# Kernel tuning notes

Measured on AMD Instinct MI355X. Metric: run time of the kernel, lower is better.

Reference implementation:

```python
import jax, jax.numpy as jnp
import numpy as np

NH = 8       # num attention heads (hardcoded in module)
NL = 6       # n_layers
EPS = 1e-5   # LayerNorm eps (torch default)


def pos_enc(dim, length):
    # faithful to module's positional_encoding: even cols sin, odd cols cos,
    # with angle = pos / 10000^(2i/dim) where i indexes ALL columns via arange(0,2*dim,2)/dim
    pos = jnp.arange(length, dtype=jnp.float32)[:, None]
    div = 1.0 / (10000.0 ** (jnp.arange(0, 2 * dim, 2, dtype=jnp.float32) / dim))
    ang = pos * div[None, :]  # [length, dim]
    cols = jnp.arange(dim)
    return jnp.where(cols % 2 == 0, jnp.sin(ang), jnp.cos(ang))


def layernorm(x):
    m = x.mean(-1, keepdims=True)
    v = x.var(-1, keepdims=True)  # biased, matches torch LayerNorm
    return (x - m) / jnp.sqrt(v + EPS)


def setup_inputs() -> dict:
    key = jax.random.key(0)
    ks = jax.random.split(key, 8)
    S, H = 2048, 1024
    D = H // NH
    sc = 1.0 / np.sqrt(H)  # ~ torch Linear init scale
    return {
        "inputs": jax.random.normal(ks[0], (S, H), jnp.float32),
        "Wq": jax.random.normal(ks[1], (NH, H, D), jnp.float32) * sc,
        "bq": jnp.zeros((NH, D), jnp.float32),
        "Wk": jax.random.normal(ks[2], (NH, H, D), jnp.float32) * sc,
        "bk": jnp.zeros((NH, D), jnp.float32),
        "Wv": jax.random.normal(ks[3], (NH, H, D), jnp.float32) * sc,
        "bv": jnp.zeros((NH, D), jnp.float32),
        "W1": jax.random.normal(ks[4], (H, H), jnp.float32) * sc,
        "b1": jnp.zeros((H,), jnp.float32),
        "W2": jax.random.normal(ks[5], (H, H), jnp.float32) * sc,
        "b2": jnp.zeros((H,), jnp.float32),
    }


def reference(inputs, Wq, bq, Wk, bk, Wv, bv, W1, b1, W2, b2):
    S, H = inputs.shape
    scale = jnp.sqrt(jnp.float32(H))  # module scales by sqrt(hidden), not sqrt(head_dim)
    x = inputs + pos_enc(H, S)        # [S, H]
    kv = x  # dropout in eval mode = identity; k_v_input fixed to layer-0 input (faithful)
    # K/V are identical every layer (shared weights + fixed kv input)
    K = jnp.einsum('sh,nhd->nsd', kv, Wk) + bk[:, None, :]  # [NH, S, D]
    V = jnp.einsum('sh,nhd->nsd', kv, Wv) + bv[:, None, :]
    t_in = x
    for _ in range(NL):
        Q = jnp.einsum('sh,nhd->nsd', t_in, Wq) + bq[:, None, :]
        A = jax.nn.softmax(jnp.einsum('nsd,ntd->nst', Q, K) / scale, axis=-1)
        ctx = jnp.einsum('nst,ntd->nsd', A, V)        # [NH, S, D]
        cat = ctx.transpose(1, 0, 2).reshape(S, H)    # concat heads on feature dim
        mh = layernorm(t_in + cat)
        ff = jax.nn.relu(mh @ W1 + b1) @ W2 + b2
        t_in = layernorm(mh + ff)
    return t_in
```

## Files before the change

### kernel.cpp

```cpp
#include <hip/hip_runtime.h>

#define S_LEN 2048
#define H_DIM 1024
#define NHEAD 8
#define D_HEAD 128
#define KSPLIT 2
#define KV_PER (S_LEN / KSPLIT)

typedef __bf16 bf16x8 __attribute__((ext_vector_type(8)));
typedef float floatx4 __attribute__((ext_vector_type(4)));

__device__ __forceinline__ float b2f(unsigned short u) {
    union { unsigned int i; float f; } v;
    v.i = ((unsigned int)u) << 16;
    return v.f;
}
__device__ __forceinline__ unsigned short f2b(float f) {
    union { float f; unsigned int i; } v;
    v.f = f;
    return (unsigned short)((v.i + 0x7fffu + ((v.i >> 16) & 1u)) >> 16);
}

__device__ __forceinline__ void dma16(void* lds, const void* g) {
    __builtin_amdgcn_global_load_lds(
        (const __attribute__((address_space(1))) void*)g,
        (__attribute__((address_space(3))) void*)lds, 16, 0, 0);
}

__global__ __launch_bounds__(256) void posenc_kernel(
    const float* __restrict__ in, float* __restrict__ xf,
    unsigned short* __restrict__ xb)
{
    int g = blockIdx.x * 256 + threadIdx.x;
    int s = g >> 10;
    int h = g & 1023;
    float dv = powf(10000.0f, -(float)h * (1.0f / 512.0f));
    float ang = (float)s * dv;
    float pe = (h & 1) ? cosf(ang) : sinf(ang);
    float x = in[g] + pe;
    xf[g] = x;
    xb[g] = f2b(x);
}

__global__ __launch_bounds__(256) void transpose_all(
    const float* __restrict__ Wq, const float* __restrict__ Wk,
    const float* __restrict__ Wv, const float* __restrict__ W1,
    const float* __restrict__ W2,
    unsigned short* __restrict__ WqT, unsigned short* __restrict__ WkT,
    unsigned short* __restrict__ WvT, unsigned short* __restrict__ W1T,
    unsigned short* __restrict__ W2T)
{
    __shared__ unsigned short tile[32][33];
    const int z = blockIdx.z;
    const float* ih;
    unsigned short* oh;
    int ldin;
    if (z < 8)       { ih = Wq + (size_t)z * 131072;        oh = WqT + (size_t)z * 131072;        ldin = 128; }
    else if (z < 16) { ih = Wk + (size_t)(z - 8) * 131072;  oh = WkT + (size_t)(z - 8) * 131072;  ldin = 128; }
    else if (z < 24) { ih = Wv + (size_t)(z - 16) * 131072; oh = WvT + (size_t)(z - 16) * 131072; ldin = 128; }
    else if (z < 32) { ih = W1 + (size_t)(z - 24) * 128;    oh = W1T + (size_t)(z - 24) * 131072; ldin = 1024; }
    else             { ih = W2 + (size_t)(z - 32) * 128;    oh = W2T + (size_t)(z - 32) * 131072; ldin = 1024; }
    const int r0 = blockIdx.y * 32, c0 = blockIdx.x * 32;
    const int tx = threadIdx.x, ty = threadIdx.y;
    for (int i = ty; i < 32; i += 8)
        tile[i][tx] = f2b(ih[(size_t)(r0 + i) * ldin + c0 + tx]);
    __syncthreads();
    for (int i = ty; i < 32; i += 8)
        oh[(size_t)(c0 + i) * 1024 + r0 + tx] = tile[tx][i];
}

template <int MODE, bool RELU>
__device__ __forceinline__ void gemm128_core(
    unsigned short* sA, unsigned short* sB,
    const unsigned short* A, const unsigned short* Bt,
    const float* bias, float* Cf, unsigned short* Cb, int ldt, int i0, int j0)
{
    const int K = H_DIM;
    const int tid = threadIdx.x;
    const int wave = tid >> 6, lane = tid & 63;
    const int quad = lane >> 4, l16 = lane & 15;
    const int wm = (wave >> 1) * 64, wn = (wave & 1) * 64;

    const int srow = lane >> 3;
    const int schunk = (lane & 7) ^ srow;
    const unsigned short* Ap = A + (size_t)(i0 + wave * 8 + srow) * K + schunk * 8;
    const unsigned short* Bp = Bt + (size_t)(j0 + wave * 8 + srow) * K + schunk * 8;

    floatx4 z4 = {0.f, 0.f, 0.f, 0.f};
    floatx4 acc[4][4];
#pragma unroll
    for (int i = 0; i < 4; i++)
#pragma unroll
        for (int j = 0; j < 4; j++) acc[i][j] = z4;

#pragma unroll
    for (int it = 0; it < 4; it++) {
        const int lb = (wave * 8 + it * 32) * 64;
        dma16(sA + lb, Ap + (size_t)(it * 32) * K);
        dma16(sB + lb, Bp + (size_t)(it * 32) * K);
    }
    __syncthreads();

    int buf = 0;
    for (int k0 = 0; k0 < K; k0 += 64) {
        if (k0 + 64 < K) {
            unsigned short* nA = sA + (buf ^ 1) * 8192;
            unsigned short* nB = sB + (buf ^ 1) * 8192;
#pragma unroll
            for (int it = 0; it < 4; it++) {
                const int lb = (wave * 8 + it * 32) * 64;
                dma16(nA + lb, Ap + (size_t)(it * 32) * K + k0 + 64);
                dma16(nB + lb, Bp + (size_t)(it * 32) * K + k0 + 64);
            }
        }
        const unsigned short* cA = sA + buf * 8192;
        const unsigned short* cB = sB + buf * 8192;
#pragma unroll
        for (int kh = 0; kh < 2; kh++) {
            bf16x8 af[4], bfr[4];
#pragma unroll
            for (int mi = 0; mi < 4; mi++) {
                int row = wm + mi * 16 + l16;
                int p = (kh * 4 + quad) ^ (l16 & 7);
                af[mi] = *(const bf16x8*)(cA + row * 64 + p * 8);
            }
#pragma unroll
            for (int ni = 0; ni < 4; ni++) {
                int row = wn + ni * 16 + l16;
                int p = (kh * 4 + quad) ^ (l16 & 7);
                bfr[ni] = *(const bf16x8*)(cB + row * 64 + p * 8);
            }
#pragma unroll
            for (int mi = 0; mi < 4; mi++)
#pragma unroll
                for (int ni = 0; ni < 4; ni++)
                    acc[mi][ni] = __builtin_amdgcn_mfma_f32_16x16x32_bf16(
                        af[mi], bfr[ni], acc[mi][ni], 0, 0, 0);
        }
        __syncthreads();
        buf ^= 1;
    }

#pragma unroll
    for (int mi = 0; mi < 4; mi++) {
#pragma unroll
        for (int ni = 0; ni < 4; ni++) {
            const int col = j0 + wn + ni * 16 + l16;
            const float bval = bias[col];
#pragma unroll
            for (int r = 0; r < 4; r++) {
                const int row_o = i0 + wm + mi * 16 + quad * 4 + r;
                float v = acc[mi][ni][r] + bval;
                if (RELU) v = fmaxf(v, 0.0f);
                if (MODE == 0) Cb[(size_t)row_o * H_DIM + col] = f2b(v);
                else if (MODE == 1) Cb[(size_t)col * ldt + row_o] = f2b(v);
                else Cf[(size_t)row_o * H_DIM + col] = v;
            }
        }
    }
}

template <int MODE, bool RELU>
__global__ __launch_bounds__(256, 2) void gemm128(
    const unsigned short* __restrict__ A, const unsigned short* __restrict__ Bt,
    const float* __restrict__ bias, float* __restrict__ Cf,
    unsigned short* __restrict__ Cb, int ldt)
{
    extern __shared__ __align__(16) unsigned short gsm[];
    gemm128_core<MODE, RELU>(gsm, gsm + 16384, A, Bt, bias, Cf, Cb, ldt,
                             blockIdx.y * 128, blockIdx.x * 128);
}

__global__ __launch_bounds__(256, 2) void gemm_kv(
    const unsigned short* __restrict__ A,
    const unsigned short* __restrict__ WkT, const unsigned short* __restrict__ WvT,
    const float* __restrict__ bk, const float* __restrict__ bv,
    unsigned short* __restrict__ Kb, unsigned short* __restrict__ Vtb)
{
    extern __shared__ __align__(16) unsigned short gsm[];
    if (blockIdx.z == 0)
        gemm128_core<0, false>(gsm, gsm + 16384, A, WkT, bk, nullptr, Kb, 0,
                               blockIdx.y * 128, blockIdx.x * 128);
    else
        gemm128_core<1, false>(gsm, gsm + 16384, A, WvT, bv, nullptr, Vtb, S_LEN,
                               blockIdx.y * 128, blockIdx.x * 128);
}

__global__ __launch_bounds__(256, 2) void flash_attn(
    const unsigned short* __restrict__ Qg, const unsigned short* __restrict__ Kg,
    const unsigned short* __restrict__ Vt, unsigned short* __restrict__ Op,
    float* __restrict__ Lp)
{
    extern __shared__ __align__(16) unsigned short smem[];
    unsigned short* sK0 = smem;
    unsigned short* sV0 = smem + 16384;
    unsigned short* sP = smem + 32768;

    const int tid = threadIdx.x;
    const int wave = tid >> 6, lane = tid & 63;
    const int quad = lane >> 4, l16 = lane & 15;
    const int head = blockIdx.y;
    const int q0 = blockIdx.x * 64;
    const int split = blockIdx.z;
    const int h0 = head * D_HEAD;

    bf16x8 aq[4];
    const int qrow = q0 + wave * 16 + l16;
#pragma unroll
    for (int ks = 0; ks < 4; ks++)
        aq[ks] = *(const bf16x8*)(Qg + (size_t)qrow * H_DIM + h0 + ks * 32 + quad * 8);

    unsigned short* myP = sP + wave * (16 * 72);

    const int k_r = wave * 4 + (lane >> 4);
    const int k_c = (lane & 15) ^ (k_r & 15);
    const int v_r = wave * 8 + (lane >> 3);
    const int v_c = (lane & 7) ^ (v_r & 7);

    const unsigned short* Kbase = Kg + h0;
    const unsigned short* Vbase = Vt + (size_t)h0 * S_LEN;
    const int kt0 = split * KV_PER;

    floatx4 z4 = {0.f, 0.f, 0.f, 0.f};
    floatx4 o[8];
#pragma unroll
    for (int i = 0; i < 8; i++) o[i] = z4;
    float l_r[4] = {0.f, 0.f, 0.f, 0.f};

#pragma unroll
    for (int it = 0; it < 4; it++) {
        dma16(sK0 + (wave * 4 + it * 16) * 128,
              Kbase + (size_t)(kt0 + k_r + it * 16) * H_DIM + k_c * 8);
        dma16(sV0 + (wave * 8 + it * 32) * 64,
              Vbase + (size_t)(v_r + it * 32) * S_LEN + kt0 + v_c * 8);
    }
    __syncthreads();

    int buf = 0;
    for (int it0 = 0; it0 < KV_PER; it0 += 64) {
        const int t0 = kt0 + it0;
        if (it0 + 64 < KV_PER) {
            const int nt = t0 + 64;
            unsigned short* nK = sK0 + (buf ^ 1) * 8192;
            unsigned short* nV = sV0 + (buf ^ 1) * 8192;
#pragma unroll
            for (int it = 0; it < 4; it++) {
                dma16(nK + (wave * 4 + it * 16) * 128,
                      Kbase + (size_t)(nt + k_r + it * 16) * H_DIM + k_c * 8);
                dma16(nV + (wave * 8 + it * 32) * 64,
                      Vbase + (size_t)(v_r + it * 32) * S_LEN + nt + v_c * 8);
            }
        }
        const unsigned short* cK = sK0 + buf * 8192;
        const unsigned short* cV = sV0 + buf * 8192;

        floatx4 sc[4];
#pragma unroll
        for (int ni = 0; ni < 4; ni++) {
            sc[ni] = z4;
#pragma unroll
            for (int ks = 0; ks < 4; ks++) {
                int p = (ks * 4 + quad) ^ l16;
                bf16x8 bk = *(const bf16x8*)(cK + (ni * 16 + l16) * 128 + p * 8);
                sc[ni] = __builtin_amdgcn_mfma_f32_16x16x32_bf16(aq[ks], bk, sc[ni], 0, 0, 0);
            }
        }

#pragma unroll
        for (int ni = 0; ni < 4; ni++)
#pragma unroll
            for (int r = 0; r < 4; r++) {
                float p = __expf(sc[ni][r] * 0.03125f);
                sc[ni][r] = p;
                l_r[r] += p;
            }

#pragma unroll
        for (int ni = 0; ni < 4; ni++)
#pragma unroll
            for (int r = 0; r < 4; r++) {
                int prow = quad * 4 + r;
                myP[prow * 72 + ((ni * 16 + l16) ^ ((prow & 8) << 1))] = f2b(sc[ni][r]);
            }
        bf16x8 ap[2];
#pragma unroll
        for (int ks = 0; ks < 2; ks++)
            ap[ks] = *(const bf16x8*)(myP + l16 * 72 + ((ks * 32 + quad * 8) ^ ((l16 & 8) << 1)));

#pragma unroll
        for (int ni = 0; ni < 8; ni++) {
#pragma unroll
            for (int ks = 0; ks < 2; ks++) {
                int p = (ks * 4 + quad) ^ (l16 & 7);
                bf16x8 bv = *(const bf16x8*)(cV + (ni * 16 + l16) * 64 + p * 8);
                o[ni] = __builtin_amdgcn_mfma_f32_16x16x32_bf16(ap[ks], bv, o[ni], 0, 0, 0);
            }
        }

        __syncthreads();
        buf ^= 1;
    }

#pragma unroll
    for (int r = 0; r < 4; r++)
#pragma unroll
        for (int off = 1; off < 16; off <<= 1)
            l_r[r] += __shfl_xor(l_r[r], off, 64);

#pragma unroll
    for (int r = 0; r < 4; r++) {
        float inv = 1.0f / l_r[r];
        int row = q0 + wave * 16 + quad * 4 + r;
#pragma unroll
        for (int ni = 0; ni < 8; ni++)
            Op[((size_t)split * S_LEN + row) * H_DIM + h0 + ni * 16 + l16] =
                f2b(o[ni][r] * inv);
        if (l16 == 0)
            Lp[(split * NHEAD + head) * S_LEN + row] = l_r[r];
    }
}

__global__ __launch_bounds__(256) void merge_add_layernorm(
    const float* __restrict__ t, const unsigned short* __restrict__ Op,
    const float* __restrict__ Lp,
    float* __restrict__ of, unsigned short* __restrict__ ob)
{
    __shared__ float red[8];
    const int row = blockIdx.x, tid = threadIdx.x;
    const int head = tid >> 5;
    const size_t base = (size_t)row * H_DIM + tid * 4;

    float l_s[KSPLIT];
    ushort4 os[KSPLIT];
#pragma unroll
    for (int sp = 0; sp < KSPLIT; sp++) {
        os[sp] = *(const ushort4*)(Op + ((size_t)sp * S_LEN + row) * H_DIM + tid * 4);
        l_s[sp] = Lp[(sp * NHEAD + head) * S_LEN + row];
    }
    float W = 0.f, a0 = 0.f, a1 = 0.f, a2 = 0.f, a3 = 0.f;
#pragma unroll
    for (int sp = 0; sp < KSPLIT; sp++) {
        float w = l_s[sp];
        W += w;
        a0 += w * b2f(os[sp].x);
        a1 += w * b2f(os[sp].y);
        a2 += w * b2f(os[sp].z);
        a3 += w * b2f(os[sp].w);
    }
    float inv = 1.0f / W;
    float4 x = *(const float4*)(t + base);
    float v0 = x.x + a0 * inv, v1 = x.y + a1 * inv;
    float v2 = x.z + a2 * inv, v3 = x.w + a3 * inv;

    float s = v0 + v1 + v2 + v3;
    float q = v0 * v0 + v1 * v1 + v2 * v2 + v3 * v3;
#pragma unroll
    for (int off = 32; off >= 1; off >>= 1) {
        s += __shfl_xor(s, off, 64);
        q += __shfl_xor(q, off, 64);
    }
    if ((tid & 63) == 0) { red[tid >> 6] = s; red[4 + (tid >> 6)] = q; }
    __syncthreads();
    s = red[0] + red[1] + red[2] + red[3];
    q = red[4] + red[5] + red[6] + red[7];
    const float mean = s * (1.0f / (float)H_DIM);
    const float var = q * (1.0f / (float)H_DIM) - mean * mean;
    const float rstd = rsqrtf(var + 1e-5f);
    float o0 = (v0 - mean) * rstd, o1 = (v1 - mean) * rstd;
    float o2 = (v2 - mean) * rstd, o3 = (v3 - mean) * rstd;
    *(float4*)(of + base) = make_float4(o0, o1, o2, o3);
    *(ushort4*)(ob + base) = make_ushort4(f2b(o0), f2b(o1), f2b(o2), f2b(o3));
}

__global__ __launch_bounds__(256) void add_layernorm(
    const float* __restrict__ a, const float* __restrict__ b,
    float* __restrict__ of, unsigned short* __restrict__ ob)
{
    __shared__ float red[8];
    const int row = blockIdx.x, tid = threadIdx.x;
    const size_t base = (size_t)row * H_DIM + tid * 4;
    float4 x = *(const float4*)(a + base);
    float4 y = *(const float4*)(b + base);
    float v0 = x.x + y.x, v1 = x.y + y.y, v2 = x.z + y.z, v3 = x.w + y.w;
    float s = v0 + v1 + v2 + v3;
    float q = v0 * v0 + v1 * v1 + v2 * v2 + v3 * v3;
#pragma unroll
    for (int off = 32; off >= 1; off >>= 1) {
        s += __shfl_xor(s, off, 64);
        q += __shfl_xor(q, off, 64);
    }
    if ((tid & 63) == 0) { red[tid >> 6] = s; red[4 + (tid >> 6)] = q; }
    __syncthreads();
    s = red[0] + red[1] + red[2] + red[3];
    q = red[4] + red[5] + red[6] + red[7];
    const float mean = s * (1.0f / (float)H_DIM);
    const float var = q * (1.0f / (float)H_DIM) - mean * mean;
    const float rstd = rsqrtf(var + 1e-5f);
    float o0 = (v0 - mean) * rstd, o1 = (v1 - mean) * rstd;
    float o2 = (v2 - mean) * rstd, o3 = (v3 - mean) * rstd;
    *(float4*)(of + base) = make_float4(o0, o1, o2, o3);
    *(ushort4*)(ob + base) = make_ushort4(f2b(o0), f2b(o1), f2b(o2), f2b(o3));
}

extern "C" void kernel_launch(void* const* d_in, const int* in_sizes, int n_in,
                              void* d_out, int out_size, void* d_ws, size_t ws_size,
                              hipStream_t stream)
{
    (void)in_sizes; (void)n_in; (void)out_size; (void)ws_size;
    const float* in = (const float*)d_in[0];
    const float* Wq = (const float*)d_in[1];
    const float* bq = (const float*)d_in[2];
    const float* Wk = (const float*)d_in[3];
    const float* bk = (const float*)d_in[4];
    const float* Wv = (const float*)d_in[5];
    const float* bv = (const float*)d_in[6];
    const float* W1 = (const float*)d_in[7];
    const float* b1 = (const float*)d_in[8];
    const float* W2 = (const float*)d_in[9];
    const float* b2 = (const float*)d_in[10];

    char* ws = (char*)d_ws;
    const size_t MB = 1024 * 1024;
    float* t_f32 = (float*)(ws + 0 * MB);
    float* cf_f32 = (float*)(ws + 8 * MB);
    unsigned short* t_b = (unsigned short*)(ws + 16 * MB);
    unsigned short* K_b = (unsigned short*)(ws + 20 * MB);
    unsigned short* Vt_b = (unsigned short*)(ws + 24 * MB);
    unsigned short* Q_b = (unsigned short*)(ws + 28 * MB);
    unsigned short* WqT = (unsigned short*)(ws + 32 * MB);
    unsigned short* WkT = (unsigned short*)(ws + 34 * MB);
    unsigned short* WvT = (unsigned short*)(ws + 36 * MB);
    unsigned short* W1T = (unsigned short*)(ws + 38 * MB);
    unsigned short* W2T = (unsigned short*)(ws + 40 * MB);
    unsigned short* Op = (unsigned short*)(ws + 42 * MB);
    float* Lp = (float*)(ws + 58 * MB);

    (void)hipFuncSetAttribute(reinterpret_cast<const void*>(&flash_attn),
                              hipFuncAttributeMaxDynamicSharedMemorySize, 74752);
    (void)hipFuncSetAttribute(reinterpret_cast<const void*>(&gemm128<0, false>),
                              hipFuncAttributeMaxDynamicSharedMemorySize, 65536);
    (void)hipFuncSetAttribute(reinterpret_cast<const void*>(&gemm128<0, true>),
                              hipFuncAttributeMaxDynamicSharedMemorySize, 65536);
    (void)hipFuncSetAttribute(reinterpret_cast<const void*>(&gemm128<2, false>),
                              hipFuncAttributeMaxDynamicSharedMemorySize, 65536);
    (void)hipFuncSetAttribute(reinterpret_cast<const void*>(&gemm_kv),
                              hipFuncAttributeMaxDynamicSharedMemorySize, 65536);

    transpose_all<<<dim3(4, 32, 40), dim3(32, 8), 0, stream>>>(
        Wq, Wk, Wv, W1, W2, WqT, WkT, WvT, W1T, W2T);

    posenc_kernel<<<(S_LEN * H_DIM) / 256, 256, 0, stream>>>(in, t_f32, t_b);

    dim3 gg(H_DIM / 128, S_LEN / 128);
    gemm_kv<<<dim3(8, 16, 2), 256, 65536, stream>>>(t_b, WkT, WvT, bk, bv, K_b, Vt_b);

    for (int layer = 0; layer < 6; layer++) {
        gemm128<0, false><<<gg, 256, 65536, stream>>>(t_b, WqT, bq, nullptr, Q_b, 0);
        flash_attn<<<dim3(S_LEN / 64, NHEAD, KSPLIT), 256, 74752, stream>>>(Q_b, K_b, Vt_b, Op, Lp);
        merge_add_layernorm<<<S_LEN, 256, 0, stream>>>(t_f32, Op, Lp, t_f32, t_b);
        gemm128<0, true><<<gg, 256, 65536, stream>>>(t_b, W1T, b1, nullptr, Q_b, 0);
        gemm128<2, false><<<gg, 256, 65536, stream>>>(Q_b, W2T, b2, cf_f32, nullptr, 0);
        float* of = (layer == 5) ? (float*)d_out : t_f32;
        add_layernorm<<<S_LEN, 256, 0, stream>>>(t_f32, cf_f32, of, t_b);
    }
}
```

Before: 593.9 us.

## Repartition flash attention work so waves split KV columns instead of query rows

Each wave now holds Q fragments for all 64 query rows and computes scores against its own 16 KV columns, then writes P to a shared block-wide tile. After a block barrier, each wave reads the full P tile and computes a 32-column slice of the output over all 64 rows. The aim is to cut per-wave LDS reads of K and V, since each K/V fragment is loaded once and reused across four MFMAs. In exchange it adds an extra __syncthreads per KV tile, a cross-wave reduction of row sums through LDS, more Q registers per wave and slightly more shared memory.

```diff
diff --git a/kernel.cpp b/kernel.cpp
--- a/kernel.cpp
+++ b/kernel.cpp
@@ -195,6 +195,7 @@
     unsigned short* sK0 = smem;
     unsigned short* sV0 = smem + 16384;
     unsigned short* sP = smem + 32768;
+    float* lsum = (float*)(smem + 32768 + 4608);
 
     const int tid = threadIdx.x;
     const int wave = tid >> 6, lane = tid & 63;
@@ -204,13 +205,14 @@
     const int split = blockIdx.z;
     const int h0 = head * D_HEAD;
 
-    bf16x8 aq[4];
-    const int qrow = q0 + wave * 16 + l16;
-#pragma unroll
-    for (int ks = 0; ks < 4; ks++)
-        aq[ks] = *(const bf16x8*)(Qg + (size_t)qrow * H_DIM + h0 + ks * 32 + quad * 8);
-
-    unsigned short* myP = sP + wave * (16 * 72);
+    bf16x8 aq[4][4];
+#pragma unroll
+    for (int mi = 0; mi < 4; mi++) {
+        const int qrow = q0 + mi * 16 + l16;
+#pragma unroll
+        for (int ks = 0; ks < 4; ks++)
+            aq[mi][ks] = *(const bf16x8*)(Qg + (size_t)qrow * H_DIM + h0 + ks * 32 + quad * 8);
+    }
 
     const int k_r = wave * 4 + (lane >> 4);
     const int k_c = (lane & 15) ^ (k_r & 15);
@@ -222,10 +224,16 @@
     const int kt0 = split * KV_PER;
 
     floatx4 z4 = {0.f, 0.f, 0.f, 0.f};
-    floatx4 o[8];
-#pragma unroll
-    for (int i = 0; i < 8; i++) o[i] = z4;
-    float l_r[4] = {0.f, 0.f, 0.f, 0.f};
+    floatx4 o[4][2];
+#pragma unroll
+    for (int mi = 0; mi < 4; mi++)
+#pragma unroll
+        for (int ni = 0; ni < 2; ni++) o[mi][ni] = z4;
+    float l_r[4][4];
+#pragma unroll
+    for (int mi = 0; mi < 4; mi++)
+#pragma unroll
+        for (int r = 0; r < 4; r++) l_r[mi][r] = 0.f;
 
 #pragma unroll
     for (int it = 0; it < 4; it++) {
@@ -256,44 +264,57 @@
 
         floatx4 sc[4];
 #pragma unroll
-        for (int ni = 0; ni < 4; ni++) {
-            sc[ni] = z4;
-#pragma unroll
-            for (int ks = 0; ks < 4; ks++) {
-                int p = (ks * 4 + quad) ^ l16;
-                bf16x8 bk = *(const bf16x8*)(cK + (ni * 16 + l16) * 128 + p * 8);
-                sc[ni] = __builtin_amdgcn_mfma_f32_16x16x32_bf16(aq[ks], bk, sc[ni], 0, 0, 0);
-            }
-        }
-
-#pragma unroll
-        for (int ni = 0; ni < 4; ni++)
+        for (int mi = 0; mi < 4; mi++) sc[mi] = z4;
+#pragma unroll
+        for (int ks = 0; ks < 4; ks++) {
+            int p = (ks * 4 + quad) ^ l16;
+            bf16x8 bk = *(const bf16x8*)(cK + (wave * 16 + l16) * 128 + p * 8);
+#pragma unroll
+            for (int mi = 0; mi < 4; mi++)
+                sc[mi] = __builtin_amdgcn_mfma_f32_16x16x32_bf16(
+                    aq[mi][ks], bk, sc[mi], 0, 0, 0);
+        }
+
+#pragma unroll
+        for (int mi = 0; mi < 4; mi++)
 #pragma unroll
             for (int r = 0; r < 4; r++) {
-                float p = __expf(sc[ni][r] * 0.03125f);
-                sc[ni][r] = p;
-                l_r[r] += p;
-            }
-
-#pragma unroll
-        for (int ni = 0; ni < 4; ni++)
+                float p = __expf(sc[mi][r] * 0.03125f);
+                sc[mi][r] = p;
+                l_r[mi][r] += p;
+            }
+
+#pragma unroll
+        for (int mi = 0; mi < 4; mi++)
 #pragma unroll
             for (int r = 0; r < 4; r++) {
-                int prow = quad * 4 + r;
-                myP[prow * 72 + ((ni * 16 + l16) ^ ((prow & 8) << 1))] = f2b(sc[ni][r]);
-            }
-        bf16x8 ap[2];
-#pragma unroll
-        for (int ks = 0; ks < 2; ks++)
-            ap[ks] = *(const bf16x8*)(myP + l16 * 72 + ((ks * 32 + quad * 8) ^ ((l16 & 8) << 1)));
-
-#pragma unroll
-        for (int ni = 0; ni < 8; ni++) {
+                int q = mi * 16 + quad * 4 + r;
+                sP[q * 72 + ((wave * 16 + l16) ^ ((q & 8) << 1))] = f2b(sc[mi][r]);
+            }
+        __syncthreads();
+
+        bf16x8 bv[2][2];
+#pragma unroll
+        for (int ni = 0; ni < 2; ni++)
 #pragma unroll
             for (int ks = 0; ks < 2; ks++) {
                 int p = (ks * 4 + quad) ^ (l16 & 7);
-                bf16x8 bv = *(const bf16x8*)(cV + (ni * 16 + l16) * 64 + p * 8);
-                o[ni] = __builtin_amdgcn_mfma_f32_16x16x32_bf16(ap[ks], bv, o[ni], 0, 0, 0);
+                bv[ni][ks] = *(const bf16x8*)(
+                    cV + ((wave * 2 + ni) * 16 + l16) * 64 + p * 8);
+            }
+#pragma unroll
+        for (int mi = 0; mi < 4; mi++) {
+            int q = mi * 16 + l16;
+            bf16x8 pa0 = *(const bf16x8*)(
+                sP + q * 72 + ((quad * 8) ^ ((q & 8) << 1)));
+            bf16x8 pa1 = *(const bf16x8*)(
+                sP + q * 72 + ((32 + quad * 8) ^ ((q & 8) << 1)));
+#pragma unroll
+            for (int ni = 0; ni < 2; ni++) {
+                o[mi][ni] = __builtin_amdgcn_mfma_f32_16x16x32_bf16(
+                    pa0, bv[ni][0], o[mi][ni], 0, 0, 0);
+                o[mi][ni] = __builtin_amdgcn_mfma_f32_16x16x32_bf16(
+                    pa1, bv[ni][1], o[mi][ni], 0, 0, 0);
             }
         }
 
@@ -302,22 +323,37 @@
     }
 
 #pragma unroll
-    for (int r = 0; r < 4; r++)
-#pragma unroll
-        for (int off = 1; off < 16; off <<= 1)
-            l_r[r] += __shfl_xor(l_r[r], off, 64);
-
-#pragma unroll
-    for (int r = 0; r < 4; r++) {
-        float inv = 1.0f / l_r[r];
-        int row = q0 + wave * 16 + quad * 4 + r;
-#pragma unroll
-        for (int ni = 0; ni < 8; ni++)
-            Op[((size_t)split * S_LEN + row) * H_DIM + h0 + ni * 16 + l16] =
-                f2b(o[ni][r] * inv);
-        if (l16 == 0)
-            Lp[(split * NHEAD + head) * S_LEN + row] = l_r[r];
-    }
+    for (int mi = 0; mi < 4; mi++)
+#pragma unroll
+        for (int r = 0; r < 4; r++)
+#pragma unroll
+            for (int off = 1; off < 16; off <<= 1)
+                l_r[mi][r] += __shfl_xor(l_r[mi][r], off, 64);
+
+    if (l16 == 0) {
+#pragma unroll
+        for (int mi = 0; mi < 4; mi++)
+#pragma unroll
+            for (int r = 0; r < 4; r++)
+                lsum[wave * 64 + mi * 16 + quad * 4 + r] = l_r[mi][r];
+    }
+    __syncthreads();
+
+#pragma unroll
+    for (int mi = 0; mi < 4; mi++)
+#pragma unroll
+        for (int r = 0; r < 4; r++) {
+            const int ql = mi * 16 + quad * 4 + r;
+            const float ltot = lsum[ql] + lsum[64 + ql] + lsum[128 + ql] + lsum[192 + ql];
+            const float inv = 1.0f / ltot;
+            const int row = q0 + ql;
+#pragma unroll
+            for (int ni = 0; ni < 2; ni++)
+                Op[((size_t)split * S_LEN + row) * H_DIM + h0 + (wave * 2 + ni) * 16 + l16] =
+                    f2b(o[mi][ni][r] * inv);
+            if (wave == 0 && l16 == 0)
+                Lp[(split * NHEAD + head) * S_LEN + row] = ltot;
+        }
 }
 
 __global__ __launch_bounds__(256) void merge_add_layernorm(
@@ -436,7 +472,7 @@
     float* Lp = (float*)(ws + 58 * MB);
 
     (void)hipFuncSetAttribute(reinterpret_cast<const void*>(&flash_attn),
-                              hipFuncAttributeMaxDynamicSharedMemorySize, 74752);
+                              hipFuncAttributeMaxDynamicSharedMemorySize, 75776);
     (void)hipFuncSetAttribute(reinterpret_cast<const void*>(&gemm128<0, false>),
                               hipFuncAttributeMaxDynamicSharedMemorySize, 65536);
     (void)hipFuncSetAttribute(reinterpret_cast<const void*>(&gemm128<0, true>),
@@ -456,7 +492,7 @@
 
     for (int layer = 0; layer < 6; layer++) {
         gemm128<0, false><<<gg, 256, 65536, stream>>>(t_b, WqT, bq, nullptr, Q_b, 0);
-        flash_attn<<<dim3(S_LEN / 64, NHEAD, KSPLIT), 256, 74752, stream>>>(Q_b, K_b, Vt_b, Op, Lp);
+        flash_attn<<<dim3(S_LEN / 64, NHEAD, KSPLIT), 256, 75776, stream>>>(Q_b, K_b, Vt_b, Op, Lp);
         merge_add_layernorm<<<S_LEN, 256, 0, stream>>>(t_f32, Op, Lp, t_f32, t_b);
         gemm128<0, true><<<gg, 256, 65536, stream>>>(t_b, W1T, b1, nullptr, Q_b, 0);
         gemm128<2, false><<<gg, 256, 65536, stream>>>(Q_b, W2T, b2, cf_f32, nullptr, 0);
```

After: 652.4 us. 1.1x slower.

## Split-K the Q-projection and FFN2 GEMMs, reducing partials in consumer kernels

Applied to the files above, without the earlier changes.

The Q projection and second FFN GEMM now run as split-K=2 launches of 256 blocks instead of 128, with each half writing fp32 partials. The partials are summed and biased in the consumers. Flash attention stages Q via LDS after adding both partials and bq, and a new add_layernorm3 sums the two W2 partials plus b2. This aims to fill more compute units on the 128-tile GEMMs. In exchange it adds fp32 partial-buffer writes and reads, plus an extra LDS pass and barrier in attention.

```diff
diff --git a/kernel.cpp b/kernel.cpp
--- a/kernel.cpp
+++ b/kernel.cpp
@@ -6,6 +6,7 @@
 #define D_HEAD 128
 #define KSPLIT 2
 #define KV_PER (S_LEN / KSPLIT)
+#define QP_ELEMS (S_LEN * H_DIM)
 
 typedef __bf16 bf16x8 __attribute__((ext_vector_type(8)));
 typedef float floatx4 __attribute__((ext_vector_type(4)));
@@ -69,13 +70,13 @@
         oh[(size_t)(c0 + i) * 1024 + r0 + tx] = tile[tx][i];
 }
 
-template <int MODE, bool RELU>
+template <int MODE, bool RELU, int KLEN>
 __device__ __forceinline__ void gemm128_core(
     unsigned short* sA, unsigned short* sB,
     const unsigned short* A, const unsigned short* Bt,
-    const float* bias, float* Cf, unsigned short* Cb, int ldt, int i0, int j0)
-{
-    const int K = H_DIM;
+    const float* bias, float* Cf, unsigned short* Cb, int ldt, int i0, int j0,
+    int kofs)
+{
     const int tid = threadIdx.x;
     const int wave = tid >> 6, lane = tid & 63;
     const int quad = lane >> 4, l16 = lane & 15;
@@ -83,8 +84,8 @@
 
     const int srow = lane >> 3;
     const int schunk = (lane & 7) ^ srow;
-    const unsigned short* Ap = A + (size_t)(i0 + wave * 8 + srow) * K + schunk * 8;
-    const unsigned short* Bp = Bt + (size_t)(j0 + wave * 8 + srow) * K + schunk * 8;
+    const unsigned short* Ap = A + (size_t)(i0 + wave * 8 + srow) * H_DIM + kofs + schunk * 8;
+    const unsigned short* Bp = Bt + (size_t)(j0 + wave * 8 + srow) * H_DIM + kofs + schunk * 8;
 
     floatx4 z4 = {0.f, 0.f, 0.f, 0.f};
     floatx4 acc[4][4];
@@ -96,21 +97,21 @@
 #pragma unroll
     for (int it = 0; it < 4; it++) {
         const int lb = (wave * 8 + it * 32) * 64;
-        dma16(sA + lb, Ap + (size_t)(it * 32) * K);
-        dma16(sB + lb, Bp + (size_t)(it * 32) * K);
+        dma16(sA + lb, Ap + (size_t)(it * 32) * H_DIM);
+        dma16(sB + lb, Bp + (size_t)(it * 32) * H_DIM);
     }
     __syncthreads();
 
     int buf = 0;
-    for (int k0 = 0; k0 < K; k0 += 64) {
-        if (k0 + 64 < K) {
+    for (int k0 = 0; k0 < KLEN; k0 += 64) {
+        if (k0 + 64 < KLEN) {
             unsigned short* nA = sA + (buf ^ 1) * 8192;
             unsigned short* nB = sB + (buf ^ 1) * 8192;
 #pragma unroll
             for (int it = 0; it < 4; it++) {
                 const int lb = (wave * 8 + it * 32) * 64;
-                dma16(nA + lb, Ap + (size_t)(it * 32) * K + k0 + 64);
-                dma16(nB + lb, Bp + (size_t)(it * 32) * K + k0 + 64);
+                dma16(nA + lb, Ap + (size_t)(it * 32) * H_DIM + k0 + 64);
+                dma16(nB + lb, Bp + (size_t)(it * 32) * H_DIM + k0 + 64);
             }
         }
         const unsigned short* cA = sA + buf * 8192;
@@ -146,7 +147,7 @@
 #pragma unroll
         for (int ni = 0; ni < 4; ni++) {
             const int col = j0 + wn + ni * 16 + l16;
-            const float bval = bias[col];
+            const float bval = (MODE == 3) ? 0.f : bias[col];
 #pragma unroll
             for (int r = 0; r < 4; r++) {
                 const int row_o = i0 + wm + mi * 16 + quad * 4 + r;
@@ -167,8 +168,19 @@
     unsigned short* __restrict__ Cb, int ldt)
 {
     extern __shared__ __align__(16) unsigned short gsm[];
-    gemm128_core<MODE, RELU>(gsm, gsm + 16384, A, Bt, bias, Cf, Cb, ldt,
-                             blockIdx.y * 128, blockIdx.x * 128);
+    gemm128_core<MODE, RELU, 1024>(gsm, gsm + 16384, A, Bt, bias, Cf, Cb, ldt,
+                                   blockIdx.y * 128, blockIdx.x * 128, 0);
+}
+
+__global__ __launch_bounds__(256, 2) void gemm_ks(
+    const unsigned short* __restrict__ A, const unsigned short* __restrict__ Bt,
+    float* __restrict__ Cp)
+{
+    extern __shared__ __align__(16) unsigned short gsm[];
+    float* Cf = Cp + (size_t)blockIdx.z * QP_ELEMS;
+    gemm128_core<3, false, 512>(gsm, gsm + 16384, A, Bt, nullptr, Cf, nullptr, 0,
+                                blockIdx.y * 128, blockIdx.x * 128,
+                                blockIdx.z * 512);
 }
 
 __global__ __launch_bounds__(256, 2) void gemm_kv(
@@ -179,17 +191,17 @@
 {
     extern __shared__ __align__(16) unsigned short gsm[];
     if (blockIdx.z == 0)
-        gemm128_core<0, false>(gsm, gsm + 16384, A, WkT, bk, nullptr, Kb, 0,
-                               blockIdx.y * 128, blockIdx.x * 128);
+        gemm128_core<0, false, 1024>(gsm, gsm + 16384, A, WkT, bk, nullptr, Kb, 0,
+                                     blockIdx.y * 128, blockIdx.x * 128, 0);
     else
-        gemm128_core<1, false>(gsm, gsm + 16384, A, WvT, bv, nullptr, Vtb, S_LEN,
-                               blockIdx.y * 128, blockIdx.x * 128);
+        gemm128_core<1, false, 1024>(gsm, gsm + 16384, A, WvT, bv, nullptr, Vtb, S_LEN,
+                                     blockIdx.y * 128, blockIdx.x * 128, 0);
 }
 
 __global__ __launch_bounds__(256, 2) void flash_attn(
-    const unsigned short* __restrict__ Qg, const unsigned short* __restrict__ Kg,
-    const unsigned short* __restrict__ Vt, unsigned short* __restrict__ Op,
-    float* __restrict__ Lp)
+    const float* __restrict__ Qp, const float* __restrict__ bq,
+    const unsigned short* __restrict__ Kg, const unsigned short* __restrict__ Vt,
+    unsigned short* __restrict__ Op, float* __restrict__ Lp)
 {
     extern __shared__ __align__(16) unsigned short smem[];
     unsigned short* sK0 = smem;
@@ -204,11 +216,39 @@
     const int split = blockIdx.z;
     const int h0 = head * D_HEAD;
 
+    unsigned short* LDSQ = smem;
+    {
+        const int r = tid >> 2;
+        const int cq = (tid & 3) * 32;
+        const float* q0p = Qp + (size_t)(q0 + r) * H_DIM + h0 + cq;
+        const float* q1p = q0p + QP_ELEMS;
+        const float* bqp = bq + head * D_HEAD + cq;
+#pragma unroll
+        for (int c = 0; c < 4; c++) {
+            float4 a0 = *(const float4*)(q0p + c * 8);
+            float4 a1 = *(const float4*)(q0p + c * 8 + 4);
+            float4 b0 = *(const float4*)(q1p + c * 8);
+            float4 b1 = *(const float4*)(q1p + c * 8 + 4);
+            float4 g0 = *(const float4*)(bqp + c * 8);
+            float4 g1 = *(const float4*)(bqp + c * 8 + 4);
+            ushort4 w0 = make_ushort4(f2b(a0.x + b0.x + g0.x), f2b(a0.y + b0.y + g0.y),
+                                      f2b(a0.z + b0.z + g0.z), f2b(a0.w + b0.w + g0.w));
+            ushort4 w1 = make_ushort4(f2b(a1.x + b1.x + g1.x), f2b(a1.y + b1.y + g1.y),
+                                      f2b(a1.z + b1.z + g1.z), f2b(a1.w + b1.w + g1.w));
+            *(ushort4*)(LDSQ + r * 136 + cq + c * 8) = w0;
+            *(ushort4*)(LDSQ + r * 136 + cq + c * 8 + 4) = w1;
+        }
+    }
+    __syncthreads();
+
     bf16x8 aq[4];
-    const int qrow = q0 + wave * 16 + l16;
-#pragma unroll
-    for (int ks = 0; ks < 4; ks++)
-        aq[ks] = *(const bf16x8*)(Qg + (size_t)qrow * H_DIM + h0 + ks * 32 + quad * 8);
+    {
+        const int qr = wave * 16 + l16;
+#pragma unroll
+        for (int ks = 0; ks < 4; ks++)
+            aq[ks] = *(const bf16x8*)(LDSQ + qr * 136 + ks * 32 + quad * 8);
+    }
+    __syncthreads();
 
     unsigned short* myP = sP + wave * (16 * 72);
 
@@ -372,16 +412,20 @@
     *(ushort4*)(ob + base) = make_ushort4(f2b(o0), f2b(o1), f2b(o2), f2b(o3));
 }
 
-__global__ __launch_bounds__(256) void add_layernorm(
-    const float* __restrict__ a, const float* __restrict__ b,
+__global__ __launch_bounds__(256) void add_layernorm3(
+    const float* __restrict__ a, const float* __restrict__ c2,
+    const float* __restrict__ b2,
     float* __restrict__ of, unsigned short* __restrict__ ob)
 {
     __shared__ float red[8];
     const int row = blockIdx.x, tid = threadIdx.x;
     const size_t base = (size_t)row * H_DIM + tid * 4;
     float4 x = *(const float4*)(a + base);
-    float4 y = *(const float4*)(b + base);
-    float v0 = x.x + y.x, v1 = x.y + y.y, v2 = x.z + y.z, v3 = x.w + y.w;
+    float4 y0 = *(const float4*)(c2 + base);
+    float4 y1 = *(const float4*)(c2 + QP_ELEMS + base);
+    float4 bb = *(const float4*)(b2 + tid * 4);
+    float v0 = x.x + y0.x + y1.x + bb.x, v1 = x.y + y0.y + y1.y + bb.y;
+    float v2 = x.z + y0.z + y1.z + bb.z, v3 = x.w + y0.w + y1.w + bb.w;
     float s = v0 + v1 + v2 + v3;
     float q = v0 * v0 + v1 * v1 + v2 * v2 + v3 * v3;
 #pragma unroll
@@ -422,26 +466,25 @@
     char* ws = (char*)d_ws;
     const size_t MB = 1024 * 1024;
     float* t_f32 = (float*)(ws + 0 * MB);
-    float* cf_f32 = (float*)(ws + 8 * MB);
-    unsigned short* t_b = (unsigned short*)(ws + 16 * MB);
-    unsigned short* K_b = (unsigned short*)(ws + 20 * MB);
-    unsigned short* Vt_b = (unsigned short*)(ws + 24 * MB);
-    unsigned short* Q_b = (unsigned short*)(ws + 28 * MB);
-    unsigned short* WqT = (unsigned short*)(ws + 32 * MB);
-    unsigned short* WkT = (unsigned short*)(ws + 34 * MB);
-    unsigned short* WvT = (unsigned short*)(ws + 36 * MB);
-    unsigned short* W1T = (unsigned short*)(ws + 38 * MB);
-    unsigned short* W2T = (unsigned short*)(ws + 40 * MB);
-    unsigned short* Op = (unsigned short*)(ws + 42 * MB);
-    float* Lp = (float*)(ws + 58 * MB);
+    unsigned short* t_b = (unsigned short*)(ws + 8 * MB);
+    unsigned short* K_b = (unsigned short*)(ws + 12 * MB);
+    unsigned short* Vt_b = (unsigned short*)(ws + 16 * MB);
+    unsigned short* F1_b = (unsigned short*)(ws + 20 * MB);
+    unsigned short* WqT = (unsigned short*)(ws + 24 * MB);
+    unsigned short* WkT = (unsigned short*)(ws + 26 * MB);
+    unsigned short* WvT = (unsigned short*)(ws + 28 * MB);
+    unsigned short* W1T = (unsigned short*)(ws + 30 * MB);
+    unsigned short* W2T = (unsigned short*)(ws + 32 * MB);
+    unsigned short* Op = (unsigned short*)(ws + 34 * MB);
+    float* Lp = (float*)(ws + 42 * MB);
+    float* Qp = (float*)(ws + 43 * MB);
+    float* C2p = (float*)(ws + 59 * MB);
 
     (void)hipFuncSetAttribute(reinterpret_cast<const void*>(&flash_attn),
                               hipFuncAttributeMaxDynamicSharedMemorySize, 74752);
-    (void)hipFuncSetAttribute(reinterpret_cast<const void*>(&gemm128<0, false>),
-                              hipFuncAttributeMaxDynamicSharedMemorySize, 65536);
     (void)hipFuncSetAttribute(reinterpret_cast<const void*>(&gemm128<0, true>),
                               hipFuncAttributeMaxDynamicSharedMemorySize, 65536);
-    (void)hipFuncSetAttribute(reinterpret_cast<const void*>(&gemm128<2, false>),
+    (void)hipFuncSetAttribute(reinterpret_cast<const void*>(&gemm_ks),
                               hipFuncAttributeMaxDynamicSharedMemorySize, 65536);
     (void)hipFuncSetAttribute(reinterpret_cast<const void*>(&gemm_kv),
                               hipFuncAttributeMaxDynamicSharedMemorySize, 65536);
@@ -451,16 +494,18 @@
 
     posenc_kernel<<<(S_LEN * H_DIM) / 256, 256, 0, stream>>>(in, t_f32, t_b);
 
+    gemm_kv<<<dim3(8, 16, 2), 256, 65536, stream>>>(t_b, WkT, WvT, bk, bv, K_b, Vt_b);
+
     dim3 gg(H_DIM / 128, S_LEN / 128);
-    gemm_kv<<<dim3(8, 16, 2), 256, 65536, stream>>>(t_b, WkT, WvT, bk, bv, K_b, Vt_b);
-
+    dim3 gk(H_DIM / 128, S_LEN / 128, 2);
     for (int layer = 0; layer < 6; layer++) {
-        gemm128<0, false><<<gg, 256, 65536, stream>>>(t_b, WqT, bq, nullptr, Q_b, 0);
-        flash_attn<<<dim3(S_LEN / 64, NHEAD, KSPLIT), 256, 74752, stream>>>(Q_b, K_b, Vt_b, Op, Lp);
+        gemm_ks<<<gk, 256, 65536, stream>>>(t_b, WqT, Qp);
+        flash_attn<<<dim3(S_LEN / 64, NHEAD, KSPLIT), 256, 74752, stream>>>(
+            Qp, bq, K_b, Vt_b, Op, Lp);
         merge_add_layernorm<<<S_LEN, 256, 0, stream>>>(t_f32, Op, Lp, t_f32, t_b);
-        gemm128<0, true><<<gg, 256, 65536, stream>>>(t_b, W1T, b1, nullptr, Q_b, 0);
-        gemm128<2, false><<<gg, 256, 65536, stream>>>(Q_b, W2T, b2, cf_f32, nullptr, 0);
+        gemm128<0, true><<<gg, 256, 65536, stream>>>(t_b, W1T, b1, nullptr, F1_b, 0);
+        gemm_ks<<<gk, 256, 65536, stream>>>(F1_b, W2T, C2p);
         float* of = (layer == 5) ? (float*)d_out : t_f32;
-        add_layernorm<<<S_LEN, 256, 0, stream>>>(t_f32, cf_f32, of, t_b);
-    }
-}
+        add_layernorm3<<<S_LEN, 256, 0, stream>>>(t_f32, C2p, b2, of, t_b);
+    }
+}
```

Measured after the change: 613.8 us. 3.3% more time.
